# Optimization experiments

Hardware: AMD Instinct MI355X
Metric: run time of the kernel (lower is better)

Reference implementation:

```python
import jax, jax.numpy as jnp
import numpy as np

PATCH = 768
POS = 64
HID = 512
B, N = 8, 2048


def setup_inputs() -> dict:
    key = jax.random.key(0)
    ks = jax.random.split(key, 8)
    d_in = PATCH + POS
    s = 1.0 / np.sqrt(d_in)
    return {
        "patches": jax.random.normal(ks[0], (B, N, PATCH), jnp.float32),
        "positions": jax.random.normal(ks[1], (B, N, POS), jnp.float32),
        "Wq": jax.random.uniform(ks[2], (d_in, HID), jnp.float32, -s, s),
        "bq": jax.random.uniform(ks[3], (HID,), jnp.float32, -s, s),
        "Wk": jax.random.uniform(ks[4], (d_in, HID), jnp.float32, -s, s),
        "bk": jax.random.uniform(ks[5], (d_in and HID,), jnp.float32, -s, s),
        "Wv": jax.random.uniform(ks[6], (d_in, HID), jnp.float32, -s, s),
        "bv": jax.random.uniform(ks[7], (HID,), jnp.float32, -s, s),
    }


def reference(patches, positions, Wq, bq, Wk, bk, Wv, bv):
    # concat patch features with positional features: [B, N, PATCH+POS]
    x = jnp.concatenate([patches, positions], axis=-1)
    Q = x @ Wq + bq  # [B, N, HID]
    K = x @ Wk + bk
    V = x @ Wv + bv
    scale = jnp.sqrt(jnp.asarray(HID, x.dtype))
    scores = jnp.einsum("bnd,bmd->bnm", Q, K) / scale  # [B, N, N]
    weights = jax.nn.softmax(scores, axis=-1)
    return jnp.einsum("bnm,bmd->bnd", weights, V)  # [B, N, HID]
```

## Files before the change

kernel.cpp:

```cpp
#include <hip/hip_runtime.h>
#include <hip/hip_bf16.h>
#include <math.h>

typedef __hip_bfloat16 bf16;
typedef __attribute__((ext_vector_type(4))) float f32x4;
typedef __attribute__((ext_vector_type(8))) short s16x8;

typedef const __attribute__((address_space(1))) void gvoid_t;
typedef __attribute__((address_space(3))) void lvoid_t;

__device__ __forceinline__ void gload16(const void* g, void* l) {
  __builtin_amdgcn_global_load_lds((gvoid_t*)g, (lvoid_t*)l, 16, 0, 0);
}
__device__ __forceinline__ unsigned short f2b(float f) {
  bf16 h = __float2bfloat16(f);
  return *(unsigned short*)&h;
}

__global__ __launch_bounds__(256) void prep_x(const float* __restrict__ patches,
                                              const float* __restrict__ positions,
                                              bf16* __restrict__ xb) {
  const long long row = blockIdx.x;
  const int c = threadIdx.x;
  const bool lo = (c < 192);
  const bool hi = (c >= 192) && (c < 208);
  const float* src = lo ? (patches + row * 768 + c * 4)
                        : (positions + row * 64 + (c - 192) * 4);
  if (lo || hi) {
    float4 v = *(const float4*)src;
    const int dst = lo ? (c * 4) : (768 + (c - 192) * 4);
    uint2 w;
    w.x = (unsigned int)f2b(v.x) | ((unsigned int)f2b(v.y) << 16);
    w.y = (unsigned int)f2b(v.z) | ((unsigned int)f2b(v.w) << 16);
    *(uint2*)(xb + row * 832 + dst) = w;
  }
}

__global__ __launch_bounds__(256) void prep_w(const float* __restrict__ Wq,
                                              const float* __restrict__ Wk,
                                              const float* __restrict__ Wv,
                                              bf16* __restrict__ Wt) {
  __shared__ float tile[32][33];
  const int z = blockIdx.z;
  const float* W = (z == 0) ? Wq : (z == 1) ? Wk : Wv;
  bf16* T = Wt + (long long)z * 512 * 832;
  const int n0 = blockIdx.x * 32;
  const int k0 = blockIdx.y * 32;
  const int tx = threadIdx.x, ty = threadIdx.y;
  #pragma unroll
  for (int i = 0; i < 32; i += 8)
    tile[ty + i][tx] = W[(long long)(k0 + ty + i) * 512 + n0 + tx];
  __syncthreads();
  #pragma unroll
  for (int i = 0; i < 32; i += 8)
    T[(long long)(n0 + ty + i) * 832 + k0 + tx] = __float2bfloat16(tile[tx][ty + i]);
}

__global__ __launch_bounds__(256) void gemm_qkv(
    const bf16* __restrict__ xb, const bf16* __restrict__ Wt,
    const float* __restrict__ bq, const float* __restrict__ bk,
    const float* __restrict__ bv,
    bf16* __restrict__ qk, bf16* __restrict__ vt) {
  __shared__ bf16 As[128 * 64];
  __shared__ bf16 Bs[128 * 64];
  const int tid = threadIdx.x;
  const int wave = tid >> 6, lane = tid & 63;
  const int llo = lane & 15, lhi = lane >> 4;
  const int wm = wave >> 1, wn = wave & 1;

  const unsigned int lin = blockIdx.x;
  const unsigned int xcd = lin & 7u, idx = lin >> 3;
  const unsigned int g = xcd * 192u + idx;
  const unsigned int bm_t = g / 12u;
  const unsigned int bn_t = g - bm_t * 12u;
  const int row0 = (int)bm_t * 128;
  const int col0 = (int)bn_t * 128;
  const int z = col0 >> 9;

  f32x4 acc[4][4] = {};

  for (int kt = 0; kt < 832; kt += 64) {
    #pragma unroll
    for (int i = 0; i < 4; i++) {
      const int c = i * 256 + tid;
      const int r = c >> 3, cc = c & 7;
      const int kk = (cc ^ (r & 7)) << 3;
      gload16(xb + ((long long)(row0 + r) * 832 + kt + kk),
              (char*)As + (long long)(i * 256 + wave * 64) * 16);
      gload16(Wt + ((long long)(col0 + r) * 832 + kt + kk),
              (char*)Bs + (long long)(i * 256 + wave * 64) * 16);
    }
    __syncthreads();
    #pragma unroll
    for (int k0 = 0; k0 < 64; k0 += 32) {
      const int xk = ((((k0 >> 3) + lhi) ^ (llo & 7)) << 3);
      s16x8 af[4], bfr[4];
      #pragma unroll
      for (int mf = 0; mf < 4; mf++)
        af[mf] = *(const s16x8*)&As[(wm * 64 + mf * 16 + llo) * 64 + xk];
      #pragma unroll
      for (int nf = 0; nf < 4; nf++)
        bfr[nf] = *(const s16x8*)&Bs[(wn * 64 + nf * 16 + llo) * 64 + xk];
      #pragma unroll
      for (int mf = 0; mf < 4; mf++)
        #pragma unroll
        for (int nf = 0; nf < 4; nf++)
          acc[mf][nf] = __builtin_amdgcn_mfma_f32_16x16x32_bf16(
              af[mf], bfr[nf], acc[mf][nf], 0, 0, 0);
    }
    __syncthreads();
  }

  if (z < 2) {
    const float* bias = z ? bk : bq;
    bf16* outp = qk + (long long)z * 16384 * 512;
    #pragma unroll
    for (int mf = 0; mf < 4; mf++)
      #pragma unroll
      for (int nf = 0; nf < 4; nf++) {
        const int c = (col0 & 511) + wn * 64 + nf * 16 + llo;
        const int grow0 = row0 + wm * 64 + mf * 16 + lhi * 4;
        const float bb = bias[c];
        #pragma unroll
        for (int r = 0; r < 4; r++)
          outp[(long long)(grow0 + r) * 512 + c] =
              __float2bfloat16(acc[mf][nf][r] + bb);
      }
  } else {
    #pragma unroll
    for (int mf = 0; mf < 4; mf++)
      #pragma unroll
      for (int nf = 0; nf < 4; nf++) {
        const int c = (col0 & 511) + wn * 64 + nf * 16 + llo;
        const int grow0 = row0 + wm * 64 + mf * 16 + lhi * 4;
        const int b = grow0 >> 11, j = grow0 & 2047;
        const float bb = bv[c];
        uint2 w;
        w.x = (unsigned int)f2b(acc[mf][nf][0] + bb) |
              ((unsigned int)f2b(acc[mf][nf][1] + bb) << 16);
        w.y = (unsigned int)f2b(acc[mf][nf][2] + bb) |
              ((unsigned int)f2b(acc[mf][nf][3] + bb) << 16);
        *(uint2*)(vt + (long long)b * 512 * 2048 + (long long)c * 2048 + j) = w;
      }
  }
}

__global__ __launch_bounds__(256) void gemm_scores(const bf16* __restrict__ qk,
                                                   bf16* __restrict__ S,
                                                   float* __restrict__ rowsumP) {
  __shared__ bf16 As[128 * 64];
  __shared__ bf16 Bs[128 * 64];
  __shared__ float psum[4][64];
  const int tid = threadIdx.x;
  const int wave = tid >> 6, lane = tid & 63;
  const int llo = lane & 15, lhi = lane >> 4;
  const int wm = wave >> 1, wn = wave & 1;

  const unsigned int lin = blockIdx.x;
  const unsigned int xcd = lin & 7u, idx = lin >> 3;
  const unsigned int g = xcd * 256u + idx;
  const int b = (int)(g >> 8);
  const unsigned int rem = g & 255u;
  const int row0 = (int)(rem >> 4) * 128;
  const int coltile = (int)(rem & 15u);
  const int col0 = coltile * 128;

  const bf16* Ab = qk + (long long)b * 2048 * 512;
  const bf16* Bb = qk + (long long)16384 * 512 + (long long)b * 2048 * 512;

  f32x4 acc[4][4] = {};
  for (int kt = 0; kt < 512; kt += 64) {
    #pragma unroll
    for (int i = 0; i < 4; i++) {
      const int c = i * 256 + tid;
      const int r = c >> 3, cc = c & 7;
      const int kk = (cc ^ (r & 7)) << 3;
      gload16(Ab + ((long long)(row0 + r) * 512 + kt + kk),
              (char*)As + (long long)(i * 256 + wave * 64) * 16);
      gload16(Bb + ((long long)(col0 + r) * 512 + kt + kk),
              (char*)Bs + (long long)(i * 256 + wave * 64) * 16);
    }
    __syncthreads();
    #pragma unroll
    for (int k0 = 0; k0 < 64; k0 += 32) {
      const int xk = ((((k0 >> 3) + lhi) ^ (llo & 7)) << 3);
      s16x8 af[4], bfr[4];
      #pragma unroll
      for (int mf = 0; mf < 4; mf++)
        af[mf] = *(const s16x8*)&As[(wm * 64 + mf * 16 + llo) * 64 + xk];
      #pragma unroll
      for (int nf = 0; nf < 4; nf++)
        bfr[nf] = *(const s16x8*)&Bs[(wn * 64 + nf * 16 + llo) * 64 + xk];
      #pragma unroll
      for (int mf = 0; mf < 4; mf++)
        #pragma unroll
        for (int nf = 0; nf < 4; nf++)
          acc[mf][nf] = __builtin_amdgcn_mfma_f32_16x16x32_bf16(
              af[mf], bfr[nf], acc[mf][nf], 0, 0, 0);
    }
    __syncthreads();
  }

  const float alpha = 0.044194173824159216f;
  #pragma unroll
  for (int mf = 0; mf < 4; mf++)
    #pragma unroll
    for (int nf = 0; nf < 4; nf++)
      #pragma unroll
      for (int r = 0; r < 4; r++)
        acc[mf][nf][r] = __expf(acc[mf][nf][r] * alpha);

  bf16* Sb = S + (long long)b * 2048 * 2048;
  #pragma unroll
  for (int mf = 0; mf < 4; mf++)
    #pragma unroll
    for (int nf = 0; nf < 4; nf++) {
      const int gcol = col0 + wn * 64 + nf * 16 + llo;
      const int grow0 = row0 + wm * 64 + mf * 16 + lhi * 4;
      #pragma unroll
      for (int r = 0; r < 4; r++)
        Sb[(long long)(grow0 + r) * 2048 + gcol] =
            __float2bfloat16(acc[mf][nf][r]);
    }

  #pragma unroll
  for (int mf = 0; mf < 4; mf++) {
    #pragma unroll
    for (int r = 0; r < 4; r++) {
      float p = acc[mf][0][r] + acc[mf][1][r] + acc[mf][2][r] + acc[mf][3][r];
      p += __shfl_xor(p, 1, 64);
      p += __shfl_xor(p, 2, 64);
      p += __shfl_xor(p, 4, 64);
      p += __shfl_xor(p, 8, 64);
      if (llo == 0) psum[wave][mf * 16 + lhi * 4 + r] = p;
    }
  }
  __syncthreads();
  if (tid < 128) {
    const int wmx = tid >> 6, i = tid & 63;
    const float v = psum[wmx * 2][i] + psum[wmx * 2 + 1][i];
    rowsumP[((long long)(b * 16 + coltile)) * 2048 + row0 + wmx * 64 + i] = v;
  }
}

__global__ __launch_bounds__(256) void reduce_rowsum(
    const float* __restrict__ rowsumP, float* __restrict__ rinv) {
  const int i = blockIdx.x * 256 + threadIdx.x;
  const int b = i >> 11, row = i & 2047;
  const float* p = rowsumP + ((long long)b * 16) * 2048 + row;
  float s = 0.f;
  #pragma unroll
  for (int t = 0; t < 16; t++) s += p[t * 2048];
  rinv[i] = 1.0f / s;
}

__global__ __launch_bounds__(256) void gemm_pv(const bf16* __restrict__ S,
                                               const bf16* __restrict__ vt,
                                               const float* __restrict__ rinv,
                                               float* __restrict__ out) {
  __shared__ bf16 As[128 * 64];
  __shared__ bf16 Bs[128 * 64];
  const int tid = threadIdx.x;
  const int wave = tid >> 6, lane = tid & 63;
  const int llo = lane & 15, lhi = lane >> 4;
  const int wm = wave >> 1, wn = wave & 1;

  const unsigned int lin = blockIdx.x;
  const unsigned int xcd = lin & 7u, idx = lin >> 3;
  const int b = (int)xcd;
  const int row0 = (int)(idx >> 2) * 128;
  const int col0 = (int)(idx & 3u) * 128;

  const bf16* Ab = S + (long long)b * 2048 * 2048;
  const bf16* Bb = vt + (long long)b * 512 * 2048;

  f32x4 acc[4][4] = {};
  for (int kt = 0; kt < 2048; kt += 64) {
    #pragma unroll
    for (int i = 0; i < 4; i++) {
      const int c = i * 256 + tid;
      const int r = c >> 3, cc = c & 7;
      const int kk = (cc ^ (r & 7)) << 3;
      gload16(Ab + ((long long)(row0 + r) * 2048 + kt + kk),
              (char*)As + (long long)(i * 256 + wave * 64) * 16);
      gload16(Bb + ((long long)(col0 + r) * 2048 + kt + kk),
              (char*)Bs + (long long)(i * 256 + wave * 64) * 16);
    }
    __syncthreads();
    #pragma unroll
    for (int k0 = 0; k0 < 64; k0 += 32) {
      const int xk = ((((k0 >> 3) + lhi) ^ (llo & 7)) << 3);
      s16x8 af[4], bfr[4];
      #pragma unroll
      for (int mf = 0; mf < 4; mf++)
        af[mf] = *(const s16x8*)&As[(wm * 64 + mf * 16 + llo) * 64 + xk];
      #pragma unroll
      for (int nf = 0; nf < 4; nf++)
        bfr[nf] = *(const s16x8*)&Bs[(wn * 64 + nf * 16 + llo) * 64 + xk];
      #pragma unroll
      for (int mf = 0; mf < 4; mf++)
        #pragma unroll
        for (int nf = 0; nf < 4; nf++)
          acc[mf][nf] = __builtin_amdgcn_mfma_f32_16x16x32_bf16(
              af[mf], bfr[nf], acc[mf][nf], 0, 0, 0);
    }
    __syncthreads();
  }

  const float* rs = rinv + (long long)b * 2048;
  float* Ob = out + (long long)b * 2048 * 512;
  #pragma unroll
  for (int mf = 0; mf < 4; mf++) {
    const int grow0 = row0 + wm * 64 + mf * 16 + lhi * 4;
    float iv[4];
    #pragma unroll
    for (int r = 0; r < 4; r++) iv[r] = rs[grow0 + r];
    #pragma unroll
    for (int nf = 0; nf < 4; nf++) {
      const int gcol = col0 + wn * 64 + nf * 16 + llo;
      #pragma unroll
      for (int r = 0; r < 4; r++)
        Ob[(long long)(grow0 + r) * 512 + gcol] = acc[mf][nf][r] * iv[r];
    }
  }
}

extern "C" void kernel_launch(void* const* d_in, const int* in_sizes, int n_in,
                              void* d_out, int out_size, void* d_ws, size_t ws_size,
                              hipStream_t stream) {
  const float* patches = (const float*)d_in[0];
  const float* positions = (const float*)d_in[1];
  const float* Wq = (const float*)d_in[2];
  const float* bq = (const float*)d_in[3];
  const float* Wk = (const float*)d_in[4];
  const float* bk = (const float*)d_in[5];
  const float* Wv = (const float*)d_in[6];
  const float* bv = (const float*)d_in[7];
  float* out = (float*)d_out;

  if (ws_size < 149422080u) return;

  char* ws = (char*)d_ws;
  bf16* Wt = (bf16*)(ws);
  bf16* xb = (bf16*)(ws + 2555904);
  bf16* qk = (bf16*)(ws + 29818880);
  bf16* vt = (bf16*)(ws + 63373312);
  bf16* S  = (bf16*)(ws + 80150528);
  float* rinv    = (float*)(ws + 147259392);
  float* rowsumP = (float*)(ws + 147324928);

  prep_x<<<16384, 256, 0, stream>>>(patches, positions, xb);
  prep_w<<<dim3(16, 26, 3), dim3(32, 8), 0, stream>>>(Wq, Wk, Wv, Wt);
  gemm_qkv<<<1536, 256, 0, stream>>>(xb, Wt, bq, bk, bv, qk, vt);
  gemm_scores<<<2048, 256, 0, stream>>>(qk, S, rowsumP);
  reduce_rowsum<<<64, 256, 0, stream>>>(rowsumP, rinv);
  gemm_pv<<<512, 256, 0, stream>>>(S, vt, rinv, out);
}
```

Before: 272.8 us.

## Rewrite scores GEMM as 256x256 tile, double-buffered 8-wave pipelined kernel

Result: no change. 272.4 us (-0.1%).

```diff
diff --git a/kernel.cpp b/kernel.cpp
--- a/kernel.cpp
+++ b/kernel.cpp
@@ -145,101 +145,168 @@
   }
 }
 
-__global__ __launch_bounds__(256) void gemm_scores(const bf16* __restrict__ qk,
-                                                   bf16* __restrict__ S,
-                                                   float* __restrict__ rowsumP) {
-  __shared__ bf16 As[128 * 64];
-  __shared__ bf16 Bs[128 * 64];
-  __shared__ float psum[4][64];
+#define VMW8 asm volatile("s_waitcnt vmcnt(8)" ::: "memory")
+#define PBAR do { __builtin_amdgcn_s_barrier(); __builtin_amdgcn_sched_barrier(0); } while (0)
+
+__device__ __forceinline__ void stage_half(const bf16* src, char* lds) {
+  gload16(src, lds);
+  gload16(src + 64 * 512, lds + 8192);
+}
+__device__ __forceinline__ void lda4(const bf16* base, int rowbase, int llo,
+                                     int xk0, int xk1, s16x8 af[4][2]) {
+  #pragma unroll
+  for (int mf = 0; mf < 4; mf++) {
+    const bf16* p = base + (rowbase + mf * 16 + llo) * 64;
+    af[mf][0] = *(const s16x8*)(p + xk0);
+    af[mf][1] = *(const s16x8*)(p + xk1);
+  }
+}
+__device__ __forceinline__ void ldb2(const bf16* base, int rowbase, int llo,
+                                     int xk0, int xk1, s16x8 bfr[2][2]) {
+  #pragma unroll
+  for (int nf = 0; nf < 2; nf++) {
+    const bf16* p = base + (rowbase + nf * 16 + llo) * 64;
+    bfr[nf][0] = *(const s16x8*)(p + xk0);
+    bfr[nf][1] = *(const s16x8*)(p + xk1);
+  }
+}
+__device__ __forceinline__ void mma16(f32x4 acc[4][2], s16x8 af[4][2],
+                                      s16x8 bfr[2][2]) {
+  __builtin_amdgcn_s_setprio(1);
+  #pragma unroll
+  for (int mf = 0; mf < 4; mf++)
+    #pragma unroll
+    for (int nf = 0; nf < 2; nf++) {
+      acc[mf][nf] = __builtin_amdgcn_mfma_f32_16x16x32_bf16(
+          af[mf][0], bfr[nf][0], acc[mf][nf], 0, 0, 0);
+      acc[mf][nf] = __builtin_amdgcn_mfma_f32_16x16x32_bf16(
+          af[mf][1], bfr[nf][1], acc[mf][nf], 0, 0, 0);
+    }
+  __builtin_amdgcn_s_setprio(0);
+}
+
+__global__ __launch_bounds__(512, 2) void gemm_scores(const bf16* __restrict__ qk,
+                                                      bf16* __restrict__ S,
+                                                      float* __restrict__ rowsumP) {
+  __shared__ bf16 As[2][256 * 64];
+  __shared__ bf16 Bs[2][256 * 64];
   const int tid = threadIdx.x;
   const int wave = tid >> 6, lane = tid & 63;
   const int llo = lane & 15, lhi = lane >> 4;
-  const int wm = wave >> 1, wn = wave & 1;
+  const int wm = wave >> 2, wn = wave & 3;
 
   const unsigned int lin = blockIdx.x;
-  const unsigned int xcd = lin & 7u, idx = lin >> 3;
-  const unsigned int g = xcd * 256u + idx;
-  const int b = (int)(g >> 8);
-  const unsigned int rem = g & 255u;
-  const int row0 = (int)(rem >> 4) * 128;
-  const int coltile = (int)(rem & 15u);
-  const int col0 = coltile * 128;
+  const int b = (int)(lin & 7u);
+  const unsigned int idx = lin >> 3;
+  const int row0 = (int)(idx >> 3) * 256;
+  const int coltile = (int)(idx & 7u);
+  const int col0 = coltile * 256;
 
   const bf16* Ab = qk + (long long)b * 2048 * 512;
   const bf16* Bb = qk + (long long)16384 * 512 + (long long)b * 2048 * 512;
 
-  f32x4 acc[4][4] = {};
-  for (int kt = 0; kt < 512; kt += 64) {
-    #pragma unroll
-    for (int i = 0; i < 4; i++) {
-      const int c = i * 256 + tid;
-      const int r = c >> 3, cc = c & 7;
-      const int kk = (cc ^ (r & 7)) << 3;
-      gload16(Ab + ((long long)(row0 + r) * 512 + kt + kk),
-              (char*)As + (long long)(i * 256 + wave * 64) * 16);
-      gload16(Bb + ((long long)(col0 + r) * 512 + kt + kk),
-              (char*)Bs + (long long)(i * 256 + wave * 64) * 16);
-    }
-    __syncthreads();
-    #pragma unroll
-    for (int k0 = 0; k0 < 64; k0 += 32) {
-      const int xk = ((((k0 >> 3) + lhi) ^ (llo & 7)) << 3);
-      s16x8 af[4], bfr[4];
-      #pragma unroll
-      for (int mf = 0; mf < 4; mf++)
-        af[mf] = *(const s16x8*)&As[(wm * 64 + mf * 16 + llo) * 64 + xk];
-      #pragma unroll
-      for (int nf = 0; nf < 4; nf++)
-        bfr[nf] = *(const s16x8*)&Bs[(wn * 64 + nf * 16 + llo) * 64 + xk];
+  const int sr = tid >> 3;
+  const int kkofs = ((tid & 7) ^ (sr & 7)) << 3;
+  const bf16* sA = Ab + (long long)(row0 + sr) * 512 + kkofs;
+  const bf16* sB = Bb + (long long)(col0 + sr) * 512 + kkofs;
+  const int wofs = wave * 1024;
+
+  const int xk0 = ((lhi ^ (llo & 7)) << 3);
+  const int xk1 = (((4 + lhi) ^ (llo & 7)) << 3);
+
+  f32x4 acc[2][2][4][2] = {};
+  s16x8 af[4][2], bf0[2][2], bf1[2][2];
+
+  stage_half(sA, (char*)As[0] + wofs);
+  stage_half(sB, (char*)Bs[0] + wofs);
+  stage_half(sB + 128 * 512, (char*)Bs[0] + 16384 + wofs);
+  stage_half(sA + 128 * 512, (char*)As[0] + 16384 + wofs);
+  stage_half(sA + 64, (char*)As[1] + wofs);
+  stage_half(sB + 64, (char*)Bs[1] + wofs);
+  VMW8;
+  PBAR;
+
+  for (int i = 0; i < 4; ++i) {
+    const int kt1 = (2 * i + 1) * 64;
+    const int kt2 = (2 * i + 2 < 8) ? (2 * i + 2) * 64 : 448;
+    const int kt3 = (2 * i + 3 < 8) ? (2 * i + 3) * 64 : 448;
+    lda4(As[0], wm * 64, llo, xk0, xk1, af);
+    ldb2(Bs[0], wn * 32, llo, xk0, xk1, bf0);
+    stage_half(sB + 128 * 512 + kt1, (char*)Bs[1] + 16384 + wofs);
+    VMW8; PBAR;
+    mma16(acc[0][0], af, bf0);
+    ldb2(Bs[0], 128 + wn * 32, llo, xk0, xk1, bf1);
+    stage_half(sA + 128 * 512 + kt1, (char*)As[1] + 16384 + wofs);
+    VMW8; PBAR;
+    mma16(acc[0][1], af, bf1);
+    lda4(As[0], 128 + wm * 64, llo, xk0, xk1, af);
+    stage_half(sA + kt2, (char*)As[0] + wofs);
+    PBAR;
+    mma16(acc[1][0], af, bf0);
+    stage_half(sB + kt2, (char*)Bs[0] + wofs);
+    VMW8; PBAR;
+    mma16(acc[1][1], af, bf1);
+    lda4(As[1], wm * 64, llo, xk0, xk1, af);
+    ldb2(Bs[1], wn * 32, llo, xk0, xk1, bf0);
+    stage_half(sB + 128 * 512 + kt2, (char*)Bs[0] + 16384 + wofs);
+    VMW8; PBAR;
+    mma16(acc[0][0], af, bf0);
+    ldb2(Bs[1], 128 + wn * 32, llo, xk0, xk1, bf1);
+    stage_half(sA + 128 * 512 + kt2, (char*)As[0] + 16384 + wofs);
+    VMW8; PBAR;
+    mma16(acc[0][1], af, bf1);
+    lda4(As[1], 128 + wm * 64, llo, xk0, xk1, af);
+    stage_half(sA + kt3, (char*)As[1] + wofs);
+    PBAR;
+    mma16(acc[1][0], af, bf0);
+    stage_half(sB + kt3, (char*)Bs[1] + wofs);
+    VMW8; PBAR;
+    mma16(acc[1][1], af, bf1);
+  }
+
+  __syncthreads();
+
+  const float alpha = 0.044194173824159216f;
+  bf16* Sb = S + (long long)b * 2048 * 2048;
+  #pragma unroll
+  for (int qr = 0; qr < 2; qr++)
+    #pragma unroll
+    for (int qc = 0; qc < 2; qc++)
       #pragma unroll
       for (int mf = 0; mf < 4; mf++)
         #pragma unroll
-        for (int nf = 0; nf < 4; nf++)
-          acc[mf][nf] = __builtin_amdgcn_mfma_f32_16x16x32_bf16(
-              af[mf], bfr[nf], acc[mf][nf], 0, 0, 0);
-    }
-    __syncthreads();
-  }
-
-  const float alpha = 0.044194173824159216f;
-  #pragma unroll
-  for (int mf = 0; mf < 4; mf++)
-    #pragma unroll
-    for (int nf = 0; nf < 4; nf++)
-      #pragma unroll
-      for (int r = 0; r < 4; r++)
-        acc[mf][nf][r] = __expf(acc[mf][nf][r] * alpha);
-
-  bf16* Sb = S + (long long)b * 2048 * 2048;
-  #pragma unroll
-  for (int mf = 0; mf < 4; mf++)
-    #pragma unroll
-    for (int nf = 0; nf < 4; nf++) {
-      const int gcol = col0 + wn * 64 + nf * 16 + llo;
-      const int grow0 = row0 + wm * 64 + mf * 16 + lhi * 4;
-      #pragma unroll
-      for (int r = 0; r < 4; r++)
-        Sb[(long long)(grow0 + r) * 2048 + gcol] =
-            __float2bfloat16(acc[mf][nf][r]);
-    }
-
-  #pragma unroll
-  for (int mf = 0; mf < 4; mf++) {
-    #pragma unroll
-    for (int r = 0; r < 4; r++) {
-      float p = acc[mf][0][r] + acc[mf][1][r] + acc[mf][2][r] + acc[mf][3][r];
-      p += __shfl_xor(p, 1, 64);
-      p += __shfl_xor(p, 2, 64);
-      p += __shfl_xor(p, 4, 64);
-      p += __shfl_xor(p, 8, 64);
-      if (llo == 0) psum[wave][mf * 16 + lhi * 4 + r] = p;
-    }
-  }
+        for (int nf = 0; nf < 2; nf++) {
+          #pragma unroll
+          for (int r = 0; r < 4; r++)
+            acc[qr][qc][mf][nf][r] = __expf(acc[qr][qc][mf][nf][r] * alpha);
+          const int gcol = col0 + qc * 128 + wn * 32 + nf * 16 + llo;
+          const int grow0 = row0 + qr * 128 + wm * 64 + mf * 16 + lhi * 4;
+          #pragma unroll
+          for (int r = 0; r < 4; r++)
+            Sb[(long long)(grow0 + r) * 2048 + gcol] =
+                __float2bfloat16(acc[qr][qc][mf][nf][r]);
+        }
+
+  float* psum = (float*)As;
+  #pragma unroll
+  for (int qr = 0; qr < 2; qr++)
+    #pragma unroll
+    for (int mf = 0; mf < 4; mf++)
+      #pragma unroll
+      for (int r = 0; r < 4; r++) {
+        float p = acc[qr][0][mf][0][r] + acc[qr][0][mf][1][r] +
+                  acc[qr][1][mf][0][r] + acc[qr][1][mf][1][r];
+        p += __shfl_xor(p, 1, 64);
+        p += __shfl_xor(p, 2, 64);
+        p += __shfl_xor(p, 4, 64);
+        p += __shfl_xor(p, 8, 64);
+        if (llo == 0)
+          psum[wn * 256 + qr * 128 + wm * 64 + mf * 16 + lhi * 4 + r] = p;
+      }
   __syncthreads();
-  if (tid < 128) {
-    const int wmx = tid >> 6, i = tid & 63;
-    const float v = psum[wmx * 2][i] + psum[wmx * 2 + 1][i];
-    rowsumP[((long long)(b * 16 + coltile)) * 2048 + row0 + wmx * 64 + i] = v;
+  if (tid < 256) {
+    const float v = psum[tid] + psum[256 + tid] + psum[512 + tid] + psum[768 + tid];
+    rowsumP[(long long)(b * 8 + coltile) * 2048 + row0 + tid] = v;
   }
 }
 
@@ -247,10 +314,10 @@
     const float* __restrict__ rowsumP, float* __restrict__ rinv) {
   const int i = blockIdx.x * 256 + threadIdx.x;
   const int b = i >> 11, row = i & 2047;
-  const float* p = rowsumP + ((long long)b * 16) * 2048 + row;
+  const float* p = rowsumP + ((long long)b * 8) * 2048 + row;
   float s = 0.f;
   #pragma unroll
-  for (int t = 0; t < 16; t++) s += p[t * 2048];
+  for (int t = 0; t < 8; t++) s += p[t * 2048];
   rinv[i] = 1.0f / s;
 }
 
@@ -352,7 +419,7 @@
   prep_x<<<16384, 256, 0, stream>>>(patches, positions, xb);
   prep_w<<<dim3(16, 26, 3), dim3(32, 8), 0, stream>>>(Wq, Wk, Wv, Wt);
   gemm_qkv<<<1536, 256, 0, stream>>>(xb, Wt, bq, bk, bv, qk, vt);
-  gemm_scores<<<2048, 256, 0, stream>>>(qk, S, rowsumP);
+  gemm_scores<<<512, 512, 0, stream>>>(qk, S, rowsumP);
   reduce_rowsum<<<64, 256, 0, stream>>>(rowsumP, rinv);
   gemm_pv<<<512, 256, 0, stream>>>(S, vt, rinv, out);
 }
```
